# Performance work log

Measured on AMD Instinct MI355X. Metric: run time of the kernel, lower is better.

Reference implementation:

```python
import jax, jax.numpy as jnp
import numpy as np

EMBED = 1024
HEAD = 64
BLOCK = 2048
B = 8


def setup_inputs() -> dict:
    key = jax.random.key(0)
    k1, k2, k3, k4 = jax.random.split(key, 4)
    inputs = jax.random.normal(k1, (B, BLOCK, EMBED), dtype=jnp.float32)
    s = 1.0 / np.sqrt(EMBED)
    Wk = jax.random.normal(k2, (EMBED, HEAD), dtype=jnp.float32) * s
    Wq = jax.random.normal(k3, (EMBED, HEAD), dtype=jnp.float32) * s
    Wv = jax.random.normal(k4, (EMBED, HEAD), dtype=jnp.float32) * s
    return {"inputs": inputs, "Wk": Wk, "Wq": Wq, "Wv": Wv}


def reference(inputs, Wk, Wq, Wv):
    # inputs: [B, T, E]; projections (bias-free Linear)
    k = inputs @ Wk  # [B, T, H]
    q = inputs @ Wq  # [B, T, H]
    v = inputs @ Wv  # [B, T, H]
    # Faithful to source: wei = k @ q^T (NOT q @ k^T)
    wei = jnp.einsum("bth,bsh->bts", k, q) * (HEAD ** -0.5)  # [B, T, T]
    T = inputs.shape[1]
    causal = jnp.tril(jnp.ones((T, T), dtype=bool))
    wei = jnp.where(causal, wei, -jnp.inf)
    wei = jax.nn.softmax(wei, axis=-1)
    out = jnp.einsum("bts,bsh->bth", wei, v)  # [B, T, H]
    return out
```

## Files before the change

### kernel.cpp

```cpp
#include <hip/hip_runtime.h>
#include <hip/hip_bf16.h>
#include <stdint.h>


typedef __attribute__((ext_vector_type(4))) float f32x4;
typedef __attribute__((ext_vector_type(4))) short s16x4;
typedef __attribute__((ext_vector_type(8))) short s16x8;
typedef __attribute__((ext_vector_type(2))) unsigned int u32x2;
typedef __attribute__((ext_vector_type(4))) unsigned int u32x4;

__device__ __forceinline__ unsigned bf16pack(float a, float b){
    unsigned ua = __builtin_bit_cast(unsigned, a);
    unsigned ub = __builtin_bit_cast(unsigned, b);
    return ((ua + 0x8000u) >> 16) | ((ub + 0x8000u) & 0xffff0000u);
}
__device__ __forceinline__ unsigned short bf16one(float a){
    return (unsigned short)((__builtin_bit_cast(unsigned, a) + 0x8000u) >> 16);
}
__device__ __forceinline__ void gload16(const void* g, unsigned short* l){
    __builtin_amdgcn_global_load_lds((const __attribute__((address_space(1))) unsigned int*)g,
                                     (__attribute__((address_space(3))) unsigned int*)l, 16, 0, 0);
}

__global__ __launch_bounds__(256) void wprep_kernel(const float* __restrict__ Wk,
                                                    const float* __restrict__ Wq,
                                                    const float* __restrict__ Wv,
                                                    unsigned short* __restrict__ WT){
    __shared__ unsigned short lt[64][66];
    int w = blockIdx.y;
    int tr = blockIdx.x;
    const float* src = (w == 0) ? Wk : (w == 1) ? Wq : Wv;
    float scale = (w == 0) ? 0.18033688011112042f : 1.0f;
    int tid = threadIdx.x;
    int row = tid >> 2, seg = tid & 3;
    const float* g = src + (size_t)(tr * 64 + row) * 64 + seg * 16;
    unsigned short* ld = &lt[row][seg * 16];
    #pragma unroll
    for (int c = 0; c < 4; c++){
        f32x4 v = *(const f32x4*)(g + c * 4);
        u32x2 pk;
        pk[0] = bf16pack(v[0] * scale, v[1] * scale);
        pk[1] = bf16pack(v[2] * scale, v[3] * scale);
        *(u32x2*)(ld + c * 4) = pk;
    }
    __syncthreads();
    int n = tid >> 2, ks = tid & 3;
    s16x8 o0, o1;
    #pragma unroll
    for (int e = 0; e < 8; e++){
        o0[e] = (short)lt[ks * 16 + e][n];
        o1[e] = (short)lt[ks * 16 + 8 + e][n];
    }
    unsigned short* dst = WT + (size_t)(w * 64 + n) * 1024 + tr * 64 + ks * 16;
    *(s16x8*)(dst)     = o0;
    *(s16x8*)(dst + 8) = o1;
}

__global__ __launch_bounds__(256) void proj_kernel(const float* __restrict__ x,
                                                   const unsigned short* __restrict__ WT,
                                                   unsigned short* __restrict__ kb,
                                                   unsigned short* __restrict__ qb,
                                                   unsigned short* __restrict__ vT){
    __shared__ unsigned short smem[32768];
    int tid = threadIdx.x; int l = tid & 63; int w = tid >> 6;
    int lr = l & 15, lg = l >> 4;
    int row0 = blockIdx.x * 32;
    int b = row0 >> 11, t0 = row0 & 2047;
    const float* xbase = x + (size_t)row0 * 1024;

    auto stage = [&](int k0, int buf){
        #pragma unroll
        for (int t = 0; t < 2; t++){
            int i = w * 2 + t;
            int r = i * 4 + (l >> 4);
            int c = l & 15;
            gload16(xbase + (size_t)r * 1024 + k0 + ((c ^ ((r & 7) << 1)) * 4),
                    smem + buf * 4096 + i * 512);
        }
        #pragma unroll
        for (int u = 0; u < 6; u++){
            int i = w * 6 + u;
            int r = i * 8 + (l >> 3);
            int c = l & 7;
            gload16(WT + (size_t)r * 1024 + k0 + ((c ^ (r & 7)) * 8),
                    smem + 8192 + buf * 12288 + i * 512);
        }
    };

    f32x4 acc[2][3] = {};
    stage(0, 0);
    __syncthreads();
    int cur = 0;
    for (int k0 = 0; k0 < 1024; k0 += 64){
        int kn = (k0 + 64 < 1024) ? (k0 + 64) : 960;
        stage(kn, cur ^ 1);
        s16x8 af[2][2];
        #pragma unroll
        for (int mf = 0; mf < 2; mf++){
            int r = mf * 16 + lr;
            const unsigned short* xrow = smem + cur * 4096 + r * 128;
            #pragma unroll
            for (int kc = 0; kc < 2; kc++){
                int c0 = (kc * 8 + lg * 2) ^ ((r & 7) << 1);
                f32x4 v0 = *(const f32x4*)(xrow + c0 * 8);
                f32x4 v1 = *(const f32x4*)(xrow + c0 * 8 + 8);
                u32x4 pk;
                pk[0] = bf16pack(v0[0], v0[1]); pk[1] = bf16pack(v0[2], v0[3]);
                pk[2] = bf16pack(v1[0], v1[1]); pk[3] = bf16pack(v1[2], v1[3]);
                af[mf][kc] = __builtin_bit_cast(s16x8, pk);
            }
        }
        #pragma unroll
        for (int nn = 0; nn < 3; nn++){
            int r = (w * 3 + nn) * 16 + lr;
            const unsigned short* wrow = smem + 8192 + cur * 12288 + r * 64;
            s16x8 b0 = *(const s16x8*)(wrow + ((lg       ^ (r & 7)) * 8));
            s16x8 b1 = *(const s16x8*)(wrow + (((4 + lg) ^ (r & 7)) * 8));
            acc[0][nn] = __builtin_amdgcn_mfma_f32_16x16x32_bf16(af[0][0], b0, acc[0][nn], 0, 0, 0);
            acc[0][nn] = __builtin_amdgcn_mfma_f32_16x16x32_bf16(af[0][1], b1, acc[0][nn], 0, 0, 0);
            acc[1][nn] = __builtin_amdgcn_mfma_f32_16x16x32_bf16(af[1][0], b0, acc[1][nn], 0, 0, 0);
            acc[1][nn] = __builtin_amdgcn_mfma_f32_16x16x32_bf16(af[1][1], b1, acc[1][nn], 0, 0, 0);
        }
        __syncthreads();
        cur ^= 1;
    }
    #pragma unroll
    for (int mf = 0; mf < 2; mf++)
        #pragma unroll
        for (int nn = 0; nn < 3; nn++){
            int col = (w * 3 + nn) * 16 + lr;
            int row = mf * 16 + lg * 4;
            #pragma unroll
            for (int r = 0; r < 4; r++)
                smem[(row + r) * 200 + col] = bf16one(acc[mf][nn][r]);
        }
    __syncthreads();
    {
        int r2 = tid >> 3, c2 = (tid & 7) * 16;
        const unsigned short* srowp = smem + r2 * 200 + c2;
        unsigned short* dst = (c2 < 64)
            ? kb + (size_t)(b * 2048 + t0 + r2) * 64 + c2
            : qb + (size_t)(b * 2048 + t0 + r2) * 64 + (c2 - 64);
        *(s16x8*)(dst)     = *(const s16x8*)(srowp);
        *(s16x8*)(dst + 8) = *(const s16x8*)(srowp + 8);
        int h = tid >> 2, q3 = tid & 3;
        s16x8 vv;
        #pragma unroll
        for (int e = 0; e < 8; e++)
            vv[e] = smem[(q3 * 8 + e) * 200 + 128 + h];
        *(s16x8*)(vT + (size_t)(b * 64 + h) * 2048 + t0 + q3 * 8) = vv;
    }
}

template<int NS>
__global__ __launch_bounds__(256) void attn_part_kernel(const unsigned short* __restrict__ kb,
                                                        const unsigned short* __restrict__ qb,
                                                        const unsigned short* __restrict__ vT,
                                                        float* __restrict__ out,
                                                        float* __restrict__ accp,
                                                        float* __restrict__ ml){
    __shared__ unsigned short Klds[2][64 * 64];
    __shared__ unsigned short Vlds[2][64 * 64];
    int tid = threadIdx.x; int l = tid & 63; int w = tid >> 6;
    int lr = l & 15, lg = l >> 4;
    int bx = blockIdx.x;
    int b = bx & 7;
    int r9 = bx >> 3;
    int bt = 31 - (r9 / NS);
    int strip = r9 % NS;
    int t0 = bt * 64;
    int tw = t0 + w * 16;
    const unsigned short* fqp = kb + (size_t)(b * 2048 + tw + lr) * 64 + lg * 8;
    s16x8 fq0 = *(const s16x8*)(fqp);
    s16x8 fq1 = *(const s16x8*)(fqp + 32);
    const unsigned short* qbb = qb + (size_t)b * 2048 * 64;
    const unsigned short* vbb = vT + (size_t)b * 64 * 2048;

    int srhi = l >> 3;
    int schk = l & 7;
    f32x4 acc[4] = {};
    float mrun = -3.0e38f, lrun = 0.0f;

    {
        int s0 = strip * 64;
        #pragma unroll
        for (int t = 0; t < 2; t++){
            int ti = w * 2 + t;
            int row = ti * 8 + srhi;
            gload16(qbb + (size_t)(s0 + row) * 64 + ((schk ^ (row & 7)) * 8), &Klds[0][ti * 512]);
            gload16(vbb + (size_t)row * 2048 + s0 + ((schk ^ (row & 7)) * 8), &Vlds[0][ti * 512]);
        }
    }
    __syncthreads();
    int cur = 0;
    for (int c = strip; c <= bt; c += NS){
        int nc = (c + NS <= bt) ? (c + NS) : c;
        int ns0 = nc * 64;
        #pragma unroll
        for (int t = 0; t < 2; t++){
            int ti = w * 2 + t;
            int row = ti * 8 + srhi;
            gload16(qbb + (size_t)(ns0 + row) * 64 + ((schk ^ (row & 7)) * 8), &Klds[cur ^ 1][ti * 512]);
            gload16(vbb + (size_t)row * 2048 + ns0 + ((schk ^ (row & 7)) * 8), &Vlds[cur ^ 1][ti * 512]);
        }
        f32x4 Cs[4];
        #pragma unroll
        for (int n = 0; n < 4; n++){
            int r = n * 16 + lr;
            const unsigned short* ka = &Klds[cur][r * 64];
            s16x8 k0 = *(const s16x8*)(ka + ((lg       ^ (r & 7)) * 8));
            s16x8 k1 = *(const s16x8*)(ka + (((4 + lg) ^ (r & 7)) * 8));
            f32x4 z = {};
            z     = __builtin_amdgcn_mfma_f32_16x16x32_bf16(k0, fq0, z, 0, 0, 0);
            Cs[n] = __builtin_amdgcn_mfma_f32_16x16x32_bf16(k1, fq1, z, 0, 0, 0);
        }
        if (c == bt){
            #pragma unroll
            for (int n = 0; n < 4; n++)
                #pragma unroll
                for (int r = 0; r < 4; r++)
                    if (n * 16 + lg * 4 + r > w * 16 + lr) Cs[n][r] = -3.0e38f;
        }
        float pm = -3.0e38f;
        #pragma unroll
        for (int n = 0; n < 4; n++)
            #pragma unroll
            for (int r = 0; r < 4; r++) pm = fmaxf(pm, Cs[n][r]);
        pm = fmaxf(pm, __shfl_xor(pm, 16));
        pm = fmaxf(pm, __shfl_xor(pm, 32));
        float mnew;
        if (__all(pm <= mrun + 8.0f)){
            mnew = mrun;
        } else {
            mnew = fmaxf(mrun, pm);
            float scl = exp2f(mrun - mnew);
            lrun *= scl;
            #pragma unroll
            for (int h16 = 0; h16 < 4; h16++) acc[h16] *= scl;
        }
        float p[4][4]; float ps = 0.0f;
        #pragma unroll
        for (int n = 0; n < 4; n++)
            #pragma unroll
            for (int r = 0; r < 4; r++){ float e = exp2f(Cs[n][r] - mnew); p[n][r] = e; ps += e; }
        ps += __shfl_xor(ps, 16);
        ps += __shfl_xor(ps, 32);
        lrun += ps;
        mrun = mnew;
        s16x4 pb[4];
        #pragma unroll
        for (int n = 0; n < 4; n++){
            u32x2 t; t[0] = bf16pack(p[n][0], p[n][1]); t[1] = bf16pack(p[n][2], p[n][3]);
            pb[n] = __builtin_bit_cast(s16x4, t);
        }
        #pragma unroll
        for (int h16 = 0; h16 < 4; h16++){
            int r = h16 * 16 + lr;
            const unsigned short* va = &Vlds[cur][r * 64];
            #pragma unroll
            for (int sl = 0; sl < 4; sl++){
                s16x4 fv = *(const s16x4*)(va + (((sl * 2 + (lg >> 1)) ^ (r & 7)) * 8) + (lg & 1) * 4);
                acc[h16] = __builtin_amdgcn_mfma_f32_16x16x16bf16_1k(fv, pb[sl], acc[h16], 0, 0, 0);
            }
        }
        __syncthreads();
        cur ^= 1;
    }
    float* accdst = (strip == 0) ? out : (accp + (size_t)(strip - 1) * (8 * 2048 * 64));
    #pragma unroll
    for (int h16 = 0; h16 < 4; h16++)
        *(f32x4*)(accdst + (size_t)(b * 2048 + tw + lr) * 64 + h16 * 16 + lg * 4) = acc[h16];
    if (lg == 0){
        int idx = ((strip * 8 + b) * 32 + bt) * 64 + w * 16 + lr;
        ml[idx * 2]     = mrun;
        ml[idx * 2 + 1] = lrun;
    }
}

template<int NS>
__global__ __launch_bounds__(256) void attn_merge_kernel(const float* __restrict__ accp,
                                                         const float* __restrict__ ml,
                                                         float* __restrict__ out){
    int bx = blockIdx.x;
    int b = bx & 7, bt = bx >> 3;
    int tid = threadIdx.x;
    int row = tid >> 2, cg = (tid & 3) * 16;
    float m[NS], lv[NS];
    float mg = -3.0e38f;
    #pragma unroll
    for (int s = 0; s < NS; s++){
        int idx = (((s * 8 + b) * 32 + bt) * 64 + row) * 2;
        m[s] = ml[idx]; lv[s] = ml[idx + 1];
        mg = fmaxf(mg, m[s]);
    }
    float wt[NS]; float lt = 0.0f;
    #pragma unroll
    for (int s = 0; s < NS; s++){ wt[s] = exp2f(m[s] - mg); lt += lv[s] * wt[s]; }
    float inv = 1.0f / lt;
    size_t base = (size_t)(b * 2048 + bt * 64 + row) * 64 + cg;
    #pragma unroll
    for (int g = 0; g < 4; g++){
        f32x4 o = (*(const f32x4*)(out + base + g * 4)) * wt[0];
        #pragma unroll
        for (int s = 1; s < NS; s++)
            o += (*(const f32x4*)(accp + (size_t)(s - 1) * (8 * 2048 * 64) + base + g * 4)) * wt[s];
        o *= inv;
        *(f32x4*)(out + base + g * 4) = o;
    }
}

__global__ __launch_bounds__(256) void attn_kernel(const unsigned short* __restrict__ kb,
                                                   const unsigned short* __restrict__ qb,
                                                   const unsigned short* __restrict__ vT,
                                                   float* __restrict__ out){
    __shared__ unsigned short Klds[2][64 * 64];
    __shared__ unsigned short Vlds[2][64 * 64];
    int tid = threadIdx.x; int l = tid & 63; int w = tid >> 6;
    int lr = l & 15, lg = l >> 4;
    int bx = blockIdx.x;
    int b = bx & 7;
    int bt = bx >> 3;
    int t0 = bt * 64;
    int tw = t0 + w * 16;
    const unsigned short* fqp = kb + (size_t)(b * 2048 + tw + lr) * 64 + lg * 8;
    s16x8 fq0 = *(const s16x8*)(fqp);
    s16x8 fq1 = *(const s16x8*)(fqp + 32);
    const unsigned short* qbb = qb + (size_t)b * 2048 * 64;
    const unsigned short* vbb = vT + (size_t)b * 64 * 2048;
    int srhi = l >> 3;
    int schk = l & 7;
    f32x4 acc[4] = {};
    float mrun = -3.0e38f, lrun = 0.0f;
    #pragma unroll
    for (int t = 0; t < 2; t++){
        int ti = w * 2 + t;
        int row = ti * 8 + srhi;
        gload16(qbb + (size_t)row * 64 + ((schk ^ (row & 7)) * 8), &Klds[0][ti * 512]);
        gload16(vbb + (size_t)row * 2048 + ((schk ^ (row & 7)) * 8), &Vlds[0][ti * 512]);
    }
    __syncthreads();
    int cur = 0;
    for (int c = 0; c <= bt; ++c){
        int nc = (c + 1 <= bt) ? (c + 1) : bt;
        int ns0 = nc * 64;
        #pragma unroll
        for (int t = 0; t < 2; t++){
            int ti = w * 2 + t;
            int row = ti * 8 + srhi;
            gload16(qbb + (size_t)(ns0 + row) * 64 + ((schk ^ (row & 7)) * 8), &Klds[cur ^ 1][ti * 512]);
            gload16(vbb + (size_t)row * 2048 + ns0 + ((schk ^ (row & 7)) * 8), &Vlds[cur ^ 1][ti * 512]);
        }
        f32x4 Cs[4];
        #pragma unroll
        for (int n = 0; n < 4; n++){
            int r = n * 16 + lr;
            const unsigned short* ka = &Klds[cur][r * 64];
            s16x8 k0 = *(const s16x8*)(ka + ((lg       ^ (r & 7)) * 8));
            s16x8 k1 = *(const s16x8*)(ka + (((4 + lg) ^ (r & 7)) * 8));
            f32x4 z = {};
            z     = __builtin_amdgcn_mfma_f32_16x16x32_bf16(k0, fq0, z, 0, 0, 0);
            Cs[n] = __builtin_amdgcn_mfma_f32_16x16x32_bf16(k1, fq1, z, 0, 0, 0);
        }
        if (c == bt){
            #pragma unroll
            for (int n = 0; n < 4; n++)
                #pragma unroll
                for (int r = 0; r < 4; r++)
                    if (n * 16 + lg * 4 + r > w * 16 + lr) Cs[n][r] = -3.0e38f;
        }
        float pm = -3.0e38f;
        #pragma unroll
        for (int n = 0; n < 4; n++)
            #pragma unroll
            for (int r = 0; r < 4; r++) pm = fmaxf(pm, Cs[n][r]);
        pm = fmaxf(pm, __shfl_xor(pm, 16));
        pm = fmaxf(pm, __shfl_xor(pm, 32));
        float mnew = fmaxf(mrun, pm);
        float scl = exp2f(mrun - mnew);
        float p[4][4]; float ps = 0.0f;
        #pragma unroll
        for (int n = 0; n < 4; n++)
            #pragma unroll
            for (int r = 0; r < 4; r++){ float e = exp2f(Cs[n][r] - mnew); p[n][r] = e; ps += e; }
        ps += __shfl_xor(ps, 16);
        ps += __shfl_xor(ps, 32);
        lrun = lrun * scl + ps;
        mrun = mnew;
        #pragma unroll
        for (int h16 = 0; h16 < 4; h16++) acc[h16] *= scl;
        s16x4 pb[4];
        #pragma unroll
        for (int n = 0; n < 4; n++){
            u32x2 t; t[0] = bf16pack(p[n][0], p[n][1]); t[1] = bf16pack(p[n][2], p[n][3]);
            pb[n] = __builtin_bit_cast(s16x4, t);
        }
        #pragma unroll
        for (int h16 = 0; h16 < 4; h16++){
            int r = h16 * 16 + lr;
            const unsigned short* va = &Vlds[cur][r * 64];
            #pragma unroll
            for (int sl = 0; sl < 4; sl++){
                s16x4 fv = *(const s16x4*)(va + (((sl * 2 + (lg >> 1)) ^ (r & 7)) * 8) + (lg & 1) * 4);
                acc[h16] = __builtin_amdgcn_mfma_f32_16x16x16bf16_1k(fv, pb[sl], acc[h16], 0, 0, 0);
            }
        }
        __syncthreads();
        cur ^= 1;
    }
    float inv = 1.0f / lrun;
    #pragma unroll
    for (int h16 = 0; h16 < 4; h16++){
        f32x4 o = acc[h16] * inv;
        *(f32x4*)(out + (size_t)(b * 2048 + tw + lr) * 64 + h16 * 16 + lg * 4) = o;
    }
}

extern "C" void kernel_launch(void* const* d_in, const int* in_sizes, int n_in,
                              void* d_out, int out_size, void* d_ws, size_t ws_size,
                              hipStream_t stream) {
    const float* x  = (const float*)d_in[0];
    const float* Wk = (const float*)d_in[1];
    const float* Wq = (const float*)d_in[2];
    const float* Wv = (const float*)d_in[3];
    float* out = (float*)d_out;
    char* ws = (char*)d_ws;
    if (ws_size < (size_t)7 * 1024 * 1024) return;
    unsigned short* WT = (unsigned short*)(ws);
    unsigned short* kb = (unsigned short*)(ws + (1u << 20));
    unsigned short* qb = (unsigned short*)(ws + (3u << 20));
    unsigned short* vT = (unsigned short*)(ws + (5u << 20));
    hipLaunchKernelGGL(wprep_kernel, dim3(16, 3), dim3(256), 0, stream, Wk, Wq, Wv, WT);
    hipLaunchKernelGGL(proj_kernel, dim3(512), dim3(256), 0, stream, x, WT, kb, qb, vT);
    if (ws_size >= (size_t)20 * 1024 * 1024){
        float* accp = (float*)(ws + ((size_t)7 << 20));
        float* ml   = (float*)(ws + ((size_t)19 << 20));
        hipLaunchKernelGGL((attn_part_kernel<4>), dim3(1024), dim3(256), 0, stream,
                           kb, qb, vT, out, accp, ml);
        hipLaunchKernelGGL((attn_merge_kernel<4>), dim3(256), dim3(256), 0, stream,
                           accp, ml, out);
    } else if (ws_size >= (size_t)12 * 1024 * 1024){
        float* accp = (float*)(ws + ((size_t)7 << 20));
        float* ml   = (float*)(ws + ((size_t)11 << 20));
        hipLaunchKernelGGL((attn_part_kernel<2>), dim3(512), dim3(256), 0, stream,
                           kb, qb, vT, out, accp, ml);
        hipLaunchKernelGGL((attn_merge_kernel<2>), dim3(256), dim3(256), 0, stream,
                           accp, ml, out);
    } else {
        hipLaunchKernelGGL(attn_kernel, dim3(256), dim3(256), 0, stream, kb, qb, vT, out);
    }
}
```

Baseline: 47.81 us.

## Process 128-key chunks per iteration in causal attention partial kernel

```diff
diff --git a/kernel.cpp b/kernel.cpp
--- a/kernel.cpp
+++ b/kernel.cpp
@@ -159,8 +159,8 @@
                                                         float* __restrict__ out,
                                                         float* __restrict__ accp,
                                                         float* __restrict__ ml){
-    __shared__ unsigned short Klds[2][64 * 64];
-    __shared__ unsigned short Vlds[2][64 * 64];
+    __shared__ unsigned short Klds[2][128 * 64];
+    __shared__ unsigned short Vlds[2][64 * 128];
     int tid = threadIdx.x; int l = tid & 63; int w = tid >> 6;
     int lr = l & 15, lg = l >> 4;
     int bx = blockIdx.x;
@@ -176,36 +176,39 @@
     const unsigned short* qbb = qb + (size_t)b * 2048 * 64;
     const unsigned short* vbb = vT + (size_t)b * 64 * 2048;
 
-    int srhi = l >> 3;
-    int schk = l & 7;
+    int nch = (bt + 2) >> 1;
+    int jmax = nch - 1;
     f32x4 acc[4] = {};
     float mrun = -3.0e38f, lrun = 0.0f;
 
-    {
-        int s0 = strip * 64;
-        #pragma unroll
-        for (int t = 0; t < 2; t++){
-            int ti = w * 2 + t;
-            int row = ti * 8 + srhi;
-            gload16(qbb + (size_t)(s0 + row) * 64 + ((schk ^ (row & 7)) * 8), &Klds[0][ti * 512]);
-            gload16(vbb + (size_t)row * 2048 + s0 + ((schk ^ (row & 7)) * 8), &Vlds[0][ti * 512]);
-        }
-    }
+    auto stageC = [&](int j, int buf){
+        int jc = (j <= jmax) ? j : jmax;
+        int s0 = jc * 128;
+        #pragma unroll
+        for (int t = 0; t < 4; t++){
+            int i = w * 4 + t;
+            int kr = i * 8 + (l >> 3);
+            int kc = l & 7;
+            gload16(qbb + (size_t)(s0 + kr) * 64 + ((kc ^ (kr & 7)) * 8), &Klds[buf][i * 512]);
+        }
+        #pragma unroll
+        for (int t = 0; t < 4; t++){
+            int i = w * 4 + t;
+            int vr = i * 4 + (l >> 4);
+            int vc = l & 15;
+            gload16(vbb + (size_t)vr * 2048 + s0 + ((vc ^ ((vr & 7) << 1)) * 8), &Vlds[buf][i * 512]);
+        }
+    };
+
+    stageC(strip, 0);
     __syncthreads();
     int cur = 0;
-    for (int c = strip; c <= bt; c += NS){
-        int nc = (c + NS <= bt) ? (c + NS) : c;
-        int ns0 = nc * 64;
-        #pragma unroll
-        for (int t = 0; t < 2; t++){
-            int ti = w * 2 + t;
-            int row = ti * 8 + srhi;
-            gload16(qbb + (size_t)(ns0 + row) * 64 + ((schk ^ (row & 7)) * 8), &Klds[cur ^ 1][ti * 512]);
-            gload16(vbb + (size_t)row * 2048 + ns0 + ((schk ^ (row & 7)) * 8), &Vlds[cur ^ 1][ti * 512]);
-        }
-        f32x4 Cs[4];
-        #pragma unroll
-        for (int n = 0; n < 4; n++){
+    for (int j = strip; j <= jmax; j += NS){
+        stageC(j + NS, cur ^ 1);
+        int s0 = j * 128;
+        f32x4 Cs[8];
+        #pragma unroll
+        for (int n = 0; n < 8; n++){
             int r = n * 16 + lr;
             const unsigned short* ka = &Klds[cur][r * 64];
             s16x8 k0 = *(const s16x8*)(ka + ((lg       ^ (r & 7)) * 8));
@@ -214,18 +217,21 @@
             z     = __builtin_amdgcn_mfma_f32_16x16x32_bf16(k0, fq0, z, 0, 0, 0);
             Cs[n] = __builtin_amdgcn_mfma_f32_16x16x32_bf16(k1, fq1, z, 0, 0, 0);
         }
-        if (c == bt){
-            #pragma unroll
-            for (int n = 0; n < 4; n++)
+        if (j == jmax){
+            int tg = tw + lr;
+            #pragma unroll
+            for (int n = 0; n < 8; n++){
+                int sg = s0 + n * 16 + lg * 4;
                 #pragma unroll
-                for (int r = 0; r < 4; r++)
-                    if (n * 16 + lg * 4 + r > w * 16 + lr) Cs[n][r] = -3.0e38f;
+                for (int rr = 0; rr < 4; rr++)
+                    if (sg + rr > tg) Cs[n][rr] = -3.0e38f;
+            }
         }
         float pm = -3.0e38f;
         #pragma unroll
-        for (int n = 0; n < 4; n++)
-            #pragma unroll
-            for (int r = 0; r < 4; r++) pm = fmaxf(pm, Cs[n][r]);
+        for (int n = 0; n < 8; n++)
+            #pragma unroll
+            for (int rr = 0; rr < 4; rr++) pm = fmaxf(pm, Cs[n][rr]);
         pm = fmaxf(pm, __shfl_xor(pm, 16));
         pm = fmaxf(pm, __shfl_xor(pm, 32));
         float mnew;
@@ -238,28 +244,28 @@
             #pragma unroll
             for (int h16 = 0; h16 < 4; h16++) acc[h16] *= scl;
         }
-        float p[4][4]; float ps = 0.0f;
-        #pragma unroll
-        for (int n = 0; n < 4; n++)
-            #pragma unroll
-            for (int r = 0; r < 4; r++){ float e = exp2f(Cs[n][r] - mnew); p[n][r] = e; ps += e; }
+        float ps = 0.0f;
+        s16x4 pb[8];
+        #pragma unroll
+        for (int n = 0; n < 8; n++){
+            float e0 = exp2f(Cs[n][0] - mnew), e1 = exp2f(Cs[n][1] - mnew);
+            float e2 = exp2f(Cs[n][2] - mnew), e3 = exp2f(Cs[n][3] - mnew);
+            ps += (e0 + e1) + (e2 + e3);
+            u32x2 t; t[0] = bf16pack(e0, e1); t[1] = bf16pack(e2, e3);
+            pb[n] = __builtin_bit_cast(s16x4, t);
+        }
         ps += __shfl_xor(ps, 16);
         ps += __shfl_xor(ps, 32);
         lrun += ps;
         mrun = mnew;
-        s16x4 pb[4];
-        #pragma unroll
-        for (int n = 0; n < 4; n++){
-            u32x2 t; t[0] = bf16pack(p[n][0], p[n][1]); t[1] = bf16pack(p[n][2], p[n][3]);
-            pb[n] = __builtin_bit_cast(s16x4, t);
-        }
         #pragma unroll
         for (int h16 = 0; h16 < 4; h16++){
             int r = h16 * 16 + lr;
-            const unsigned short* va = &Vlds[cur][r * 64];
-            #pragma unroll
-            for (int sl = 0; sl < 4; sl++){
-                s16x4 fv = *(const s16x4*)(va + (((sl * 2 + (lg >> 1)) ^ (r & 7)) * 8) + (lg & 1) * 4);
+            const unsigned short* va = &Vlds[cur][r * 128];
+            #pragma unroll
+            for (int sl = 0; sl < 8; sl++){
+                int ch = sl * 2 + (lg >> 1);
+                s16x4 fv = *(const s16x4*)(va + ((ch ^ ((r & 7) << 1)) * 8) + (lg & 1) * 4);
                 acc[h16] = __builtin_amdgcn_mfma_f32_16x16x16bf16_1k(fv, pb[sl], acc[h16], 0, 0, 0);
             }
         }
```

Result: slower. 54.78 us (+14.6%).
